# Kernel optimization log

Hardware: AMD Instinct MI355X
Metric: run time of the kernel (lower is better)

The kernel has to match this reference:

```python
import jax, jax.numpy as jnp
import numpy as np

VOCAB = 200000
HID = 128
OUT = 5
N_LEAVES = 512  # balanced tree -> 1023 total nodes, children precede parents


def _build_tree(n_leaves):
    n = 2 * n_leaves - 1
    left = np.zeros(n, dtype=np.int32)
    right = np.zeros(n, dtype=np.int32)
    is_leaf = np.zeros(n, dtype=bool)
    is_leaf[:n_leaves] = True
    level = list(range(n_leaves))
    idx = n_leaves
    while len(level) > 1:
        nxt = []
        for a, b in zip(level[::2], level[1::2]):
            left[idx] = a
            right[idx] = b
            nxt.append(idx)
            idx += 1
        level = nxt
    return left, right, is_leaf


def setup_inputs() -> dict:
    key = jax.random.key(0)
    ks = jax.random.split(key, 7)
    left, right, is_leaf = _build_tree(N_LEAVES)
    n = left.shape[0]
    word_ids = jax.random.randint(ks[0], (n,), 0, VOCAB, dtype=jnp.int32)
    s = 0.05  # small init scale to keep tanh un-saturated; math identical
    return {
        "embed": jax.random.normal(ks[1], (VOCAB, HID), jnp.float32) * s,
        "V": jax.random.normal(ks[2], (HID, 2 * HID, 2 * HID), jnp.float32) * s,
        "W": jax.random.normal(ks[3], (2 * HID, HID), jnp.float32) * s,
        "b": jax.random.normal(ks[4], (1, HID), jnp.float32) * s,
        "W_out_w": jax.random.normal(ks[5], (OUT, HID), jnp.float32) * s,
        "W_out_b": jax.random.normal(ks[6], (OUT,), jnp.float32) * s,
        "word_ids": word_ids,
        "left": jnp.asarray(left),
        "right": jnp.asarray(right),
        "is_leaf": jnp.asarray(is_leaf),
    }


def reference(embed, V, W, b, W_out_w, W_out_b, word_ids, left, right, is_leaf):
    n = word_ids.shape[0]
    h = embed.shape[1]
    H0 = jnp.zeros((n, h), dtype=embed.dtype)

    def step(H, inp):
        t, wid, l, r, leaf = inp

        def leaf_fn():
            return embed[wid]

        def internal_fn():
            x = jnp.concatenate([H[l], H[r]])  # (2h,) concated child states
            # torch loop over V slices == einsum over stacked V: (x V_k x^T)_k
            xVx = jnp.einsum('i,kij,j->k', x, V, x)
            return jnp.tanh(xVx + x @ W + b[0])

        cur = jax.lax.cond(leaf, leaf_fn, internal_fn)
        return H.at[t].set(cur), None

    xs = (jnp.arange(n), word_ids, left, right, is_leaf)
    H, _ = jax.lax.scan(step, H0, xs)
    logits = H @ W_out_w.T + W_out_b
    return jax.nn.log_softmax(logits, axis=1)
```

## Files before the change

kernel.cpp:

```cpp
#include <hip/hip_runtime.h>
#include <math.h>

#define HID 128
#define NNODES 1023
#define NLEAVES 512

typedef __attribute__((ext_vector_type(8))) short short8;
typedef __attribute__((ext_vector_type(4))) short short4v;
typedef __attribute__((ext_vector_type(4))) float f32x4;

__device__ __forceinline__ unsigned short f2bf(float f) {
    unsigned int u = __float_as_uint(f);
    u += 0x7FFFu + ((u >> 16) & 1u);
    return (unsigned short)(u >> 16);
}
__device__ __forceinline__ float bf2f(unsigned short s) {
    return __uint_as_float(((unsigned int)s) << 16);
}
__device__ __forceinline__ void pack_hilo(float a, float c, unsigned& h, unsigned& l) {
    const unsigned short ha = f2bf(a), hc = f2bf(c);
    const unsigned short la = f2bf(a - bf2f(ha)), lc = f2bf(c - bf2f(hc));
    h = (unsigned)ha | ((unsigned)hc << 16);
    l = (unsigned)la | ((unsigned)lc << 16);
}

__global__ void conv_kernel(const float* __restrict__ V, const float* __restrict__ W,
                            unsigned short* __restrict__ Vp, float* __restrict__ Wt) {
    const int ihalf = blockIdx.x, k = blockIdx.y;
    const int t = threadIdx.x, w = t >> 6, lane = t & 63;
    const int colsel = lane & 15, kg = lane >> 4;
    const size_t srcK = (size_t)k << 16;
    const size_t dstK = (size_t)k << 17;
#pragma unroll
    for (int fi = 0; fi < 16; ++fi) {
        const int frag = w * 16 + fi, ks = frag >> 3, it = frag & 7;
        const int irow = ihalf * 128 + it * 16 + colsel;
        const int j0 = ks * 32 + kg * 8;
        const float4 s0 = *(const float4*)&V[srcK + (size_t)irow * 256 + j0];
        const float4 s1 = *(const float4*)&V[srcK + (size_t)irow * 256 + j0 + 4];
        uint4 ph, pl;
        pack_hilo(s0.x, s0.y, ph.x, pl.x);
        pack_hilo(s0.z, s0.w, ph.y, pl.y);
        pack_hilo(s1.x, s1.y, ph.z, pl.z);
        pack_hilo(s1.z, s1.w, ph.w, pl.w);
        const size_t d = dstK + (size_t)((ihalf * 8 + ks) * 8 + it) * 1024 + lane * 8;
        *(uint4*)&Vp[d] = ph;
        *(uint4*)&Vp[d + 512] = pl;
    }
    if (ihalf == 0) Wt[(size_t)k * 256 + t] = W[(size_t)t * HID + k];
}

__global__ void leaf_kernel(const float* __restrict__ embed,
                            const int* __restrict__ word_ids,
                            float* __restrict__ H) {
    const int t = blockIdx.x, h = threadIdx.x;
    H[(size_t)t * HID + h] = embed[(size_t)word_ids[t] * HID + h];
}

template<int NR>
__global__ __launch_bounds__(256, 2)
void level_mfma(const unsigned short* __restrict__ Vp, const float* __restrict__ Wt,
                const float* __restrict__ b, const int* __restrict__ left,
                const int* __restrict__ right, float* __restrict__ H,
                int levelStart, int nn) {
    constexpr int ROWS = NR * 16;
    __shared__ __align__(16) unsigned short Xh[ROWS * 256];
    __shared__ __align__(16) unsigned short Xl[ROWS * 256];
    __shared__ float qred[2 * 64 * 2];

    const int t = threadIdx.x;
    const int fl = blockIdx.x + gridDim.x * blockIdx.y;
    const int gX = gridDim.x;
    const int xcd = fl & 7, r2 = fl >> 3;
    const int gxv = r2 % gX;
    const int gyv = xcd * 8 + r2 / gX;
    const int k0 = gyv * 2;
    const int w = t >> 6, lane = t & 63;
    const int kslot = w >> 1, ihalf = w & 1;
    const int k = k0 + kslot;
    const int colsel = lane & 15, kg = lane >> 4;
    const size_t kbase = (size_t)k << 17;
    const int n0 = gxv * ROWS;

    for (int idx = t; idx < ROWS * 32; idx += 256) {
        const int row = idx >> 5, i0 = (idx & 31) * 8, n = n0 + row;
        uint4 ph = make_uint4(0u, 0u, 0u, 0u), pl = ph;
        if (n < nn) {
            const int node = levelStart + n;
            const int child = (i0 < HID) ? left[node] : right[node];
            const float4* hp = (const float4*)&H[(size_t)child * HID + (i0 & 127)];
            const float4 x0 = hp[0], x1 = hp[1];
            pack_hilo(x0.x, x0.y, ph.x, pl.x);
            pack_hilo(x0.z, x0.w, ph.y, pl.y);
            pack_hilo(x1.x, x1.y, ph.z, pl.z);
            pack_hilo(x1.z, x1.w, ph.w, pl.w);
        }
        const int ad = (row * 256 + i0) ^ ((row & 7) << 3);
        *(uint4*)&Xh[ad] = ph;
        *(uint4*)&Xl[ad] = pl;
    }
    __syncthreads();

    f32x4 acc[NR][8];
#pragma unroll
    for (int it = 0; it < 8; ++it) {
        const f32x4 wv = *(const f32x4*)&Wt[(size_t)k * 256 + ihalf * 128 + it * 16 + kg * 4];
#pragma unroll
        for (int nr = 0; nr < NR; ++nr) acc[nr][it] = wv;
    }

#pragma unroll
    for (int ks = 0; ks < 8; ++ks) {
        short8 xh[NR], xl[NR];
#pragma unroll
        for (int nr = 0; nr < NR; ++nr) {
            const int row = nr * 16 + colsel;
            const int ad = (row * 256 + ks * 32 + kg * 8) ^ ((row & 7) << 3);
            xh[nr] = *(const short8*)&Xh[ad];
            xl[nr] = *(const short8*)&Xl[ad];
        }
        const size_t fb = kbase + (size_t)((ihalf * 8 + ks) * 8) * 1024 + lane * 8;
#pragma unroll
        for (int it = 0; it < 8; ++it) {
            const short8 vh = *(const short8*)&Vp[fb + it * 1024];
            const short8 vl = *(const short8*)&Vp[fb + it * 1024 + 512];
#pragma unroll
            for (int nr = 0; nr < NR; ++nr) {
                acc[nr][it] = __builtin_amdgcn_mfma_f32_16x16x32_bf16(vh, xh[nr], acc[nr][it], 0, 0, 0);
                acc[nr][it] = __builtin_amdgcn_mfma_f32_16x16x32_bf16(vl, xh[nr], acc[nr][it], 0, 0, 0);
                acc[nr][it] = __builtin_amdgcn_mfma_f32_16x16x32_bf16(vh, xl[nr], acc[nr][it], 0, 0, 0);
            }
        }
    }

    float qp[NR];
#pragma unroll
    for (int nr = 0; nr < NR; ++nr) qp[nr] = 0.f;
#pragma unroll
    for (int it = 0; it < 8; ++it) {
        const int i0 = ihalf * 128 + it * 16 + kg * 4;
#pragma unroll
        for (int nr = 0; nr < NR; ++nr) {
            const int row = nr * 16 + colsel;
            const int ad = (row * 256 + i0) ^ ((row & 7) << 3);
            const short4v h4 = *(const short4v*)&Xh[ad];
            const short4v l4 = *(const short4v*)&Xl[ad];
#pragma unroll
            for (int r = 0; r < 4; ++r) {
                const float x = bf2f((unsigned short)h4[r]) + bf2f((unsigned short)l4[r]);
                qp[nr] = fmaf(x, acc[nr][it][r], qp[nr]);
            }
        }
    }
#pragma unroll
    for (int nr = 0; nr < NR; ++nr) {
        qp[nr] += __shfl_xor(qp[nr], 16, 64);
        qp[nr] += __shfl_xor(qp[nr], 32, 64);
    }
    if (kg == 0) {
#pragma unroll
        for (int nr = 0; nr < NR; ++nr)
            qred[(kslot * 64 + nr * 16 + colsel) * 2 + ihalf] = qp[nr];
    }
    __syncthreads();
    if (t < 128) {
        const int ksl = t >> 6, n = t & 63;
        if (n < ROWS && n0 + n < nn) {
            const float s = b[k0 + ksl] + qred[(ksl * 64 + n) * 2 + 0]
                                        + qred[(ksl * 64 + n) * 2 + 1];
            H[(size_t)(levelStart + n0 + n) * HID + (k0 + ksl)] = tanhf(s);
        }
    }
}

__global__ void out_kernel(const float* __restrict__ H,
                           const float* __restrict__ Wout,
                           const float* __restrict__ bout,
                           float* __restrict__ out) {
    const int t = blockIdx.x, l = threadIdx.x;
    const float h0 = H[(size_t)t * HID + l];
    const float h1 = H[(size_t)t * HID + 64 + l];
    float p[5];
#pragma unroll
    for (int o = 0; o < 5; ++o) {
        p[o] = h0 * Wout[o * HID + l] + h1 * Wout[o * HID + 64 + l];
#pragma unroll
        for (int m = 1; m < 64; m <<= 1) p[o] += __shfl_xor(p[o], m, 64);
    }
    if (l == 0) {
        float lg[5], mx = -1e30f;
#pragma unroll
        for (int o = 0; o < 5; ++o) { lg[o] = p[o] + bout[o]; mx = fmaxf(mx, lg[o]); }
        float s = 0.f;
#pragma unroll
        for (int o = 0; o < 5; ++o) s += expf(lg[o] - mx);
        const float lse = mx + logf(s);
#pragma unroll
        for (int o = 0; o < 5; ++o) out[(size_t)t * 5 + o] = lg[o] - lse;
    }
}

extern "C" void kernel_launch(void* const* d_in, const int* in_sizes, int n_in,
                              void* d_out, int out_size, void* d_ws, size_t ws_size,
                              hipStream_t stream) {
    const float* embed   = (const float*)d_in[0];
    const float* V       = (const float*)d_in[1];
    const float* W       = (const float*)d_in[2];
    const float* b       = (const float*)d_in[3];
    const float* Woutw   = (const float*)d_in[4];
    const float* Woutb   = (const float*)d_in[5];
    const int*   wordids = (const int*)d_in[6];
    const int*   left    = (const int*)d_in[7];
    const int*   right   = (const int*)d_in[8];

    unsigned short* Vp = (unsigned short*)d_ws;
    float* Wt  = (float*)((char*)d_ws + (size_t)128 * 131072 * 2);
    float* H   = Wt + (size_t)128 * 256;
    float* out = (float*)d_out;

    conv_kernel<<<dim3(2, 128), 256, 0, stream>>>(V, W, Vp, Wt);
    leaf_kernel<<<NLEAVES, HID, 0, stream>>>(embed, wordids, H);

    level_mfma<4><<<dim3(4, 64), 256, 0, stream>>>(Vp, Wt, b, left, right, H, 512, 256);
    level_mfma<4><<<dim3(2, 64), 256, 0, stream>>>(Vp, Wt, b, left, right, H, 768, 128);
    level_mfma<4><<<dim3(1, 64), 256, 0, stream>>>(Vp, Wt, b, left, right, H, 896,  64);
    level_mfma<2><<<dim3(1, 64), 256, 0, stream>>>(Vp, Wt, b, left, right, H, 960,  32);
    level_mfma<1><<<dim3(1, 64), 256, 0, stream>>>(Vp, Wt, b, left, right, H, 992,  16);
    level_mfma<1><<<dim3(1, 64), 256, 0, stream>>>(Vp, Wt, b, left, right, H, 1008,  8);
    level_mfma<1><<<dim3(1, 64), 256, 0, stream>>>(Vp, Wt, b, left, right, H, 1016,  4);
    level_mfma<1><<<dim3(1, 64), 256, 0, stream>>>(Vp, Wt, b, left, right, H, 1020,  2);
    level_mfma<1><<<dim3(1, 64), 256, 0, stream>>>(Vp, Wt, b, left, right, H, 1022,  1);

    out_kernel<<<NNODES, 64, 0, stream>>>(H, Woutw, Woutb, out);
}
```

Baseline: 343.7 us.

## Replace per-level launches with one persistent cooperative kernel holding V in registers

All separate kernels (V conversion, leaf copy, nine level kernels and the output kernel) are merged into a single cooperative persistent kernel with 128 blocks, one per output channel k. Each block converts its V_k slice to hi/lo bf16 once and keeps it in registers for the whole tree. Levels are separated by a software grid barrier. Leaf embeddings are read directly from the embedding table instead of being copied first. This removes repeated launch overhead and repeated V streaming from global memory, but adds grid-barrier latency, high register pressure, and only 128 blocks of parallelism on the large levels.

```diff
diff --git a/kernel.cpp b/kernel.cpp
--- a/kernel.cpp
+++ b/kernel.cpp
@@ -2,8 +2,8 @@
 #include <math.h>
 
 #define HID 128
-#define NNODES 1023
-#define NLEAVES 512
+#define NB 128
+#define NT 512
 
 typedef __attribute__((ext_vector_type(8))) short short8;
 typedef __attribute__((ext_vector_type(4))) short short4v;
@@ -24,179 +24,187 @@
     l = (unsigned)la | ((unsigned)lc << 16);
 }
 
-__global__ void conv_kernel(const float* __restrict__ V, const float* __restrict__ W,
-                            unsigned short* __restrict__ Vp, float* __restrict__ Wt) {
-    const int ihalf = blockIdx.x, k = blockIdx.y;
-    const int t = threadIdx.x, w = t >> 6, lane = t & 63;
-    const int colsel = lane & 15, kg = lane >> 4;
-    const size_t srcK = (size_t)k << 16;
-    const size_t dstK = (size_t)k << 17;
-#pragma unroll
-    for (int fi = 0; fi < 16; ++fi) {
-        const int frag = w * 16 + fi, ks = frag >> 3, it = frag & 7;
-        const int irow = ihalf * 128 + it * 16 + colsel;
-        const int j0 = ks * 32 + kg * 8;
-        const float4 s0 = *(const float4*)&V[srcK + (size_t)irow * 256 + j0];
-        const float4 s1 = *(const float4*)&V[srcK + (size_t)irow * 256 + j0 + 4];
-        uint4 ph, pl;
-        pack_hilo(s0.x, s0.y, ph.x, pl.x);
-        pack_hilo(s0.z, s0.w, ph.y, pl.y);
-        pack_hilo(s1.x, s1.y, ph.z, pl.z);
-        pack_hilo(s1.z, s1.w, ph.w, pl.w);
-        const size_t d = dstK + (size_t)((ihalf * 8 + ks) * 8 + it) * 1024 + lane * 8;
-        *(uint4*)&Vp[d] = ph;
-        *(uint4*)&Vp[d + 512] = pl;
-    }
-    if (ihalf == 0) Wt[(size_t)k * 256 + t] = W[(size_t)t * HID + k];
-}
-
-__global__ void leaf_kernel(const float* __restrict__ embed,
-                            const int* __restrict__ word_ids,
-                            float* __restrict__ H) {
-    const int t = blockIdx.x, h = threadIdx.x;
-    H[(size_t)t * HID + h] = embed[(size_t)word_ids[t] * HID + h];
-}
-
-template<int NR>
-__global__ __launch_bounds__(256, 2)
-void level_mfma(const unsigned short* __restrict__ Vp, const float* __restrict__ Wt,
-                const float* __restrict__ b, const int* __restrict__ left,
-                const int* __restrict__ right, float* __restrict__ H,
-                int levelStart, int nn) {
-    constexpr int ROWS = NR * 16;
-    __shared__ __align__(16) unsigned short Xh[ROWS * 256];
-    __shared__ __align__(16) unsigned short Xl[ROWS * 256];
-    __shared__ float qred[2 * 64 * 2];
+__device__ __forceinline__ void gridbar(unsigned* bar) {
+    __syncthreads();
+    if (threadIdx.x == 0) {
+        __threadfence();
+        unsigned* cnt = bar;
+        unsigned* gen = bar + 1;
+        unsigned g = __hip_atomic_load(gen, __ATOMIC_RELAXED, __HIP_MEMORY_SCOPE_AGENT);
+        unsigned a = __hip_atomic_fetch_add(cnt, 1u, __ATOMIC_ACQ_REL, __HIP_MEMORY_SCOPE_AGENT);
+        if (a == (unsigned)(NB - 1)) {
+            __hip_atomic_store(cnt, 0u, __ATOMIC_RELAXED, __HIP_MEMORY_SCOPE_AGENT);
+            __hip_atomic_store(gen, g + 1u, __ATOMIC_RELEASE, __HIP_MEMORY_SCOPE_AGENT);
+        } else {
+            while (__hip_atomic_load(gen, __ATOMIC_ACQUIRE, __HIP_MEMORY_SCOPE_AGENT) == g)
+                __builtin_amdgcn_s_sleep(8);
+        }
+        __threadfence();
+    }
+    __syncthreads();
+}
+
+__global__ __launch_bounds__(NT, 2)
+void rntn_persistent(const float* __restrict__ embed, const float* __restrict__ V,
+                     const float* __restrict__ W, const float* __restrict__ b,
+                     const float* __restrict__ Woutw, const float* __restrict__ Woutb,
+                     const int* __restrict__ word_ids, const int* __restrict__ left,
+                     const int* __restrict__ right, float* __restrict__ H,
+                     unsigned* bar, float* __restrict__ out)
+{
+    __shared__ __align__(16) unsigned short Xh[32 * 256];
+    __shared__ __align__(16) unsigned short Xl[32 * 256];
+    __shared__ float qred[256];
 
     const int t = threadIdx.x;
-    const int fl = blockIdx.x + gridDim.x * blockIdx.y;
-    const int gX = gridDim.x;
-    const int xcd = fl & 7, r2 = fl >> 3;
-    const int gxv = r2 % gX;
-    const int gyv = xcd * 8 + r2 / gX;
-    const int k0 = gyv * 2;
-    const int w = t >> 6, lane = t & 63;
-    const int kslot = w >> 1, ihalf = w & 1;
-    const int k = k0 + kslot;
-    const int colsel = lane & 15, kg = lane >> 4;
-    const size_t kbase = (size_t)k << 17;
-    const int n0 = gxv * ROWS;
-
-    for (int idx = t; idx < ROWS * 32; idx += 256) {
-        const int row = idx >> 5, i0 = (idx & 31) * 8, n = n0 + row;
-        uint4 ph = make_uint4(0u, 0u, 0u, 0u), pl = ph;
-        if (n < nn) {
-            const int node = levelStart + n;
-            const int child = (i0 < HID) ? left[node] : right[node];
-            const float4* hp = (const float4*)&H[(size_t)child * HID + (i0 & 127)];
-            const float4 x0 = hp[0], x1 = hp[1];
-            pack_hilo(x0.x, x0.y, ph.x, pl.x);
-            pack_hilo(x0.z, x0.w, ph.y, pl.y);
-            pack_hilo(x1.x, x1.y, ph.z, pl.z);
-            pack_hilo(x1.z, x1.w, ph.w, pl.w);
-        }
-        const int ad = (row * 256 + i0) ^ ((row & 7) << 3);
-        *(uint4*)&Xh[ad] = ph;
-        *(uint4*)&Xl[ad] = pl;
-    }
-    __syncthreads();
-
-    f32x4 acc[NR][8];
-#pragma unroll
-    for (int it = 0; it < 8; ++it) {
-        const f32x4 wv = *(const f32x4*)&Wt[(size_t)k * 256 + ihalf * 128 + it * 16 + kg * 4];
-#pragma unroll
-        for (int nr = 0; nr < NR; ++nr) acc[nr][it] = wv;
-    }
-
-#pragma unroll
-    for (int ks = 0; ks < 8; ++ks) {
-        short8 xh[NR], xl[NR];
-#pragma unroll
-        for (int nr = 0; nr < NR; ++nr) {
-            const int row = nr * 16 + colsel;
-            const int ad = (row * 256 + ks * 32 + kg * 8) ^ ((row & 7) << 3);
-            xh[nr] = *(const short8*)&Xh[ad];
-            xl[nr] = *(const short8*)&Xl[ad];
-        }
-        const size_t fb = kbase + (size_t)((ihalf * 8 + ks) * 8) * 1024 + lane * 8;
-#pragma unroll
-        for (int it = 0; it < 8; ++it) {
-            const short8 vh = *(const short8*)&Vp[fb + it * 1024];
-            const short8 vl = *(const short8*)&Vp[fb + it * 1024 + 512];
-#pragma unroll
-            for (int nr = 0; nr < NR; ++nr) {
-                acc[nr][it] = __builtin_amdgcn_mfma_f32_16x16x32_bf16(vh, xh[nr], acc[nr][it], 0, 0, 0);
-                acc[nr][it] = __builtin_amdgcn_mfma_f32_16x16x32_bf16(vl, xh[nr], acc[nr][it], 0, 0, 0);
-                acc[nr][it] = __builtin_amdgcn_mfma_f32_16x16x32_bf16(vh, xl[nr], acc[nr][it], 0, 0, 0);
-            }
-        }
-    }
-
-    float qp[NR];
-#pragma unroll
-    for (int nr = 0; nr < NR; ++nr) qp[nr] = 0.f;
-#pragma unroll
-    for (int it = 0; it < 8; ++it) {
-        const int i0 = ihalf * 128 + it * 16 + kg * 4;
-#pragma unroll
-        for (int nr = 0; nr < NR; ++nr) {
-            const int row = nr * 16 + colsel;
-            const int ad = (row * 256 + i0) ^ ((row & 7) << 3);
-            const short4v h4 = *(const short4v*)&Xh[ad];
-            const short4v l4 = *(const short4v*)&Xl[ad];
-#pragma unroll
-            for (int r = 0; r < 4; ++r) {
-                const float x = bf2f((unsigned short)h4[r]) + bf2f((unsigned short)l4[r]);
-                qp[nr] = fmaf(x, acc[nr][it][r], qp[nr]);
-            }
-        }
-    }
-#pragma unroll
-    for (int nr = 0; nr < NR; ++nr) {
-        qp[nr] += __shfl_xor(qp[nr], 16, 64);
-        qp[nr] += __shfl_xor(qp[nr], 32, 64);
-    }
-    if (kg == 0) {
-#pragma unroll
-        for (int nr = 0; nr < NR; ++nr)
-            qred[(kslot * 64 + nr * 16 + colsel) * 2 + ihalf] = qp[nr];
-    }
-    __syncthreads();
-    if (t < 128) {
-        const int ksl = t >> 6, n = t & 63;
-        if (n < ROWS && n0 + n < nn) {
-            const float s = b[k0 + ksl] + qred[(ksl * 64 + n) * 2 + 0]
-                                        + qred[(ksl * 64 + n) * 2 + 1];
-            H[(size_t)(levelStart + n0 + n) * HID + (k0 + ksl)] = tanhf(s);
-        }
-    }
-}
-
-__global__ void out_kernel(const float* __restrict__ H,
-                           const float* __restrict__ Wout,
-                           const float* __restrict__ bout,
-                           float* __restrict__ out) {
-    const int t = blockIdx.x, l = threadIdx.x;
-    const float h0 = H[(size_t)t * HID + l];
-    const float h1 = H[(size_t)t * HID + 64 + l];
-    float p[5];
-#pragma unroll
-    for (int o = 0; o < 5; ++o) {
-        p[o] = h0 * Wout[o * HID + l] + h1 * Wout[o * HID + 64 + l];
-#pragma unroll
-        for (int m = 1; m < 64; m <<= 1) p[o] += __shfl_xor(p[o], m, 64);
-    }
-    if (l == 0) {
-        float lg[5], mx = -1e30f;
-#pragma unroll
-        for (int o = 0; o < 5; ++o) { lg[o] = p[o] + bout[o]; mx = fmaxf(mx, lg[o]); }
-        float s = 0.f;
-#pragma unroll
-        for (int o = 0; o < 5; ++o) s += expf(lg[o] - mx);
-        const float lse = mx + logf(s);
-#pragma unroll
-        for (int o = 0; o < 5; ++o) out[(size_t)t * 5 + o] = lg[o] - lse;
+    const int k = blockIdx.x;
+    const int w = t >> 6;
+    const int ihalf = w >> 2;
+    const int jq = w & 3;
+    const int lane = t & 63;
+    const int colsel = lane & 15;
+    const int kg = lane >> 4;
+
+    short8 vfh[8][2], vfl[8][2];
+    {
+        const float* Vk = V + ((size_t)k << 16) + (size_t)ihalf * 128 * 256 + jq * 64;
+#pragma unroll
+        for (int ig = 0; ig < 8; ++ig) {
+#pragma unroll
+            for (int ks = 0; ks < 2; ++ks) {
+                const float* p = Vk + (size_t)(ig * 16 + colsel) * 256 + ks * 32 + kg * 8;
+                const float4 s0 = *(const float4*)p;
+                const float4 s1 = *(const float4*)(p + 4);
+                uint4 ph, pl;
+                pack_hilo(s0.x, s0.y, ph.x, pl.x);
+                pack_hilo(s0.z, s0.w, ph.y, pl.y);
+                pack_hilo(s1.x, s1.y, ph.z, pl.z);
+                pack_hilo(s1.z, s1.w, ph.w, pl.w);
+                vfh[ig][ks] = *(short8*)&ph;
+                vfl[ig][ks] = *(short8*)&pl;
+            }
+        }
+    }
+    f32x4 wk[8];
+#pragma unroll
+    for (int ig = 0; ig < 8; ++ig) {
+        const int i0 = ihalf * 128 + ig * 16 + kg * 4;
+#pragma unroll
+        for (int r = 0; r < 4; ++r) wk[ig][r] = W[(size_t)(i0 + r) * HID + k];
+    }
+    const float bk = b[k];
+
+    int ls = 512, nn = 256;
+#pragma unroll 1
+    for (int L = 0; L < 9; ++L) {
+        const int ntiles = (nn + 31) >> 5;
+#pragma unroll 1
+        for (int tile = 0; tile < ntiles; ++tile) {
+            const int nbase = tile << 5;
+            for (int idx = t; idx < 1024; idx += NT) {
+                const int row = idx >> 5, ch = idx & 31, i0 = ch * 8;
+                uint4 ph = make_uint4(0u, 0u, 0u, 0u), pl = ph;
+                const int n = nbase + row;
+                if (n < nn) {
+                    const int node = ls + n;
+                    const int child = (i0 < HID) ? left[node] : right[node];
+                    const float* src = (child < 512)
+                        ? (embed + (size_t)word_ids[child] * HID)
+                        : (H + (size_t)child * HID);
+                    const float4 x0 = *(const float4*)(src + (i0 & 127));
+                    const float4 x1 = *(const float4*)(src + (i0 & 127) + 4);
+                    pack_hilo(x0.x, x0.y, ph.x, pl.x);
+                    pack_hilo(x0.z, x0.w, ph.y, pl.y);
+                    pack_hilo(x1.x, x1.y, ph.z, pl.z);
+                    pack_hilo(x1.z, x1.w, ph.w, pl.w);
+                }
+                const int ad = (row * 256 + i0) ^ ((row & 7) << 3);
+                *(uint4*)&Xh[ad] = ph;
+                *(uint4*)&Xl[ad] = pl;
+            }
+            __syncthreads();
+
+#pragma unroll
+            for (int g = 0; g < 2; ++g) {
+                const int brow = g * 16 + colsel;
+                short8 bh[2], bl[2];
+#pragma unroll
+                for (int ks = 0; ks < 2; ++ks) {
+                    const int ad = (brow * 256 + jq * 64 + ks * 32 + kg * 8) ^ ((brow & 7) << 3);
+                    bh[ks] = *(const short8*)&Xh[ad];
+                    bl[ks] = *(const short8*)&Xl[ad];
+                }
+                f32x4 acc[8];
+#pragma unroll
+                for (int ig = 0; ig < 8; ++ig)
+                    acc[ig] = (jq == 0) ? wk[ig] : (f32x4){0.f, 0.f, 0.f, 0.f};
+#pragma unroll
+                for (int ks = 0; ks < 2; ++ks) {
+#pragma unroll
+                    for (int ig = 0; ig < 8; ++ig) {
+                        acc[ig] = __builtin_amdgcn_mfma_f32_16x16x32_bf16(vfh[ig][ks], bh[ks], acc[ig], 0, 0, 0);
+                        acc[ig] = __builtin_amdgcn_mfma_f32_16x16x32_bf16(vfl[ig][ks], bh[ks], acc[ig], 0, 0, 0);
+                        acc[ig] = __builtin_amdgcn_mfma_f32_16x16x32_bf16(vfh[ig][ks], bl[ks], acc[ig], 0, 0, 0);
+                    }
+                }
+                float q = 0.f;
+#pragma unroll
+                for (int ig = 0; ig < 8; ++ig) {
+                    const int i0 = ihalf * 128 + ig * 16 + kg * 4;
+                    const int ad = (brow * 256 + i0) ^ ((brow & 7) << 3);
+                    const short4v h4 = *(const short4v*)&Xh[ad];
+                    const short4v l4 = *(const short4v*)&Xl[ad];
+#pragma unroll
+                    for (int r = 0; r < 4; ++r) {
+                        const float xv = bf2f((unsigned short)h4[r]) + bf2f((unsigned short)l4[r]);
+                        q = fmaf(xv, acc[ig][r], q);
+                    }
+                }
+                q += __shfl_xor(q, 16, 64);
+                q += __shfl_xor(q, 32, 64);
+                if (kg == 0) qred[w * 32 + g * 16 + colsel] = q;
+            }
+            __syncthreads();
+            if (t < 32) {
+                const int n = nbase + t;
+                if (n < nn) {
+                    float s = bk;
+#pragma unroll
+                    for (int ww = 0; ww < 8; ++ww) s += qred[ww * 32 + t];
+                    H[(size_t)(ls + n) * HID + k] = tanhf(s);
+                }
+            }
+        }
+        gridbar(bar);
+        ls += nn;
+        nn >>= 1;
+    }
+
+    const int node = k * 8 + w;
+    if (node < 1023) {
+        const float* hrow = (node < 512)
+            ? (embed + (size_t)word_ids[node] * HID)
+            : (H + (size_t)node * HID);
+        const float h0 = hrow[lane];
+        const float h1 = hrow[64 + lane];
+        float p[5];
+#pragma unroll
+        for (int o = 0; o < 5; ++o) {
+            p[o] = h0 * Woutw[o * HID + lane] + h1 * Woutw[o * HID + 64 + lane];
+#pragma unroll
+            for (int m = 1; m < 64; m <<= 1) p[o] += __shfl_xor(p[o], m, 64);
+        }
+        if (lane == 0) {
+            float lg[5], mx = -1e30f;
+#pragma unroll
+            for (int o = 0; o < 5; ++o) { lg[o] = p[o] + Woutb[o]; mx = fmaxf(mx, lg[o]); }
+            float s = 0.f;
+#pragma unroll
+            for (int o = 0; o < 5; ++o) s += expf(lg[o] - mx);
+            const float lse = mx + logf(s);
+#pragma unroll
+            for (int o = 0; o < 5; ++o) out[(size_t)node * 5 + o] = lg[o] - lse;
+        }
     }
 }
 
@@ -213,23 +221,15 @@
     const int*   left    = (const int*)d_in[7];
     const int*   right   = (const int*)d_in[8];
 
-    unsigned short* Vp = (unsigned short*)d_ws;
-    float* Wt  = (float*)((char*)d_ws + (size_t)128 * 131072 * 2);
-    float* H   = Wt + (size_t)128 * 256;
-    float* out = (float*)d_out;
-
-    conv_kernel<<<dim3(2, 128), 256, 0, stream>>>(V, W, Vp, Wt);
-    leaf_kernel<<<NLEAVES, HID, 0, stream>>>(embed, wordids, H);
-
-    level_mfma<4><<<dim3(4, 64), 256, 0, stream>>>(Vp, Wt, b, left, right, H, 512, 256);
-    level_mfma<4><<<dim3(2, 64), 256, 0, stream>>>(Vp, Wt, b, left, right, H, 768, 128);
-    level_mfma<4><<<dim3(1, 64), 256, 0, stream>>>(Vp, Wt, b, left, right, H, 896,  64);
-    level_mfma<2><<<dim3(1, 64), 256, 0, stream>>>(Vp, Wt, b, left, right, H, 960,  32);
-    level_mfma<1><<<dim3(1, 64), 256, 0, stream>>>(Vp, Wt, b, left, right, H, 992,  16);
-    level_mfma<1><<<dim3(1, 64), 256, 0, stream>>>(Vp, Wt, b, left, right, H, 1008,  8);
-    level_mfma<1><<<dim3(1, 64), 256, 0, stream>>>(Vp, Wt, b, left, right, H, 1016,  4);
-    level_mfma<1><<<dim3(1, 64), 256, 0, stream>>>(Vp, Wt, b, left, right, H, 1020,  2);
-    level_mfma<1><<<dim3(1, 64), 256, 0, stream>>>(Vp, Wt, b, left, right, H, 1022,  1);
-
-    out_kernel<<<NNODES, 64, 0, stream>>>(H, Woutw, Woutb, out);
-}
+    float*    H   = (float*)d_ws;
+    unsigned* bar = (unsigned*)((char*)d_ws + (1 << 20));
+    float*    out = (float*)d_out;
+
+    hipMemsetAsync(bar, 0, 8, stream);
+
+    void* args[] = {(void*)&embed, (void*)&V, (void*)&W, (void*)&b,
+                    (void*)&Woutw, (void*)&Woutb, (void*)&wordids,
+                    (void*)&left, (void*)&right, (void*)&H, (void*)&bar, (void*)&out};
+    hipLaunchCooperativeKernel((void*)rntn_persistent, dim3(NB), dim3(NT),
+                               args, 0, stream);
+}
```

Measured after the change: 402.1 us. 17.0% more time.
